# Kernel optimization log

Measured on AMD Instinct MI355X. Metric: run time of the kernel, lower is better.

## Reference

```python
import jax, jax.numpy as jnp
import numpy as np

N_GROUPS = 32
N_HEADS = 8
GN_EPS = 1e-5


def setup_inputs() -> dict:
    key = jax.random.key(0)
    k1, k2, k3 = jax.random.split(key, 3)
    B, C, H, W = 8, 512, 32, 32
    x = jax.random.normal(k1, (B, C, H, W), dtype=jnp.float32)
    gn_w = jnp.ones((C,), dtype=jnp.float32)
    gn_b = jnp.zeros((C,), dtype=jnp.float32)
    qkv_w = jax.random.normal(k2, (3 * C, C), dtype=jnp.float32) * 0.02
    qkv_b = jnp.zeros((3 * C,), dtype=jnp.float32)
    proj_w = jax.random.normal(k3, (C, C), dtype=jnp.float32) * 0.02
    proj_b = jnp.zeros((C,), dtype=jnp.float32)
    return {"x": x, "gn_w": gn_w, "gn_b": gn_b, "qkv_w": qkv_w,
            "qkv_b": qkv_b, "proj_w": proj_w, "proj_b": proj_b}


def reference(x, gn_w, gn_b, qkv_w, qkv_b, proj_w, proj_b):
    b, c, h, w = x.shape
    t = h * w
    xf = x.reshape(b, c, t)

    # GroupNorm(32, C) over (channel-group, spatial) dims
    xg = xf.reshape(b, N_GROUPS, (c // N_GROUPS) * t)
    mean = jnp.mean(xg, axis=-1, keepdims=True)
    var = jnp.var(xg, axis=-1, keepdims=True)
    normed = ((xg - mean) * jax.lax.rsqrt(var + GN_EPS)).reshape(b, c, t)
    normed = normed * gn_w[None, :, None] + gn_b[None, :, None]

    # 1x1 Conv1d -> matmul over channel dim
    qkv = jnp.einsum('oc,bct->bot', qkv_w, normed) + qkv_b[None, :, None]
    q, k, v = jnp.split(qkv, 3, axis=1)  # each [b, c, t]

    ch = c // N_HEADS
    scale = 1.0 / np.sqrt(np.sqrt(ch)).astype(np.float32)
    q = (q * scale).reshape(b * N_HEADS, ch, t)
    k = (k * scale).reshape(b * N_HEADS, ch, t)
    v = v.reshape(b * N_HEADS, ch, t)

    weight = jnp.einsum('bct,bcs->bts', q, k)
    weight = jax.nn.softmax(weight.astype(jnp.float32), axis=-1).astype(q.dtype)
    a = jnp.einsum('bts,bcs->bct', weight, v).reshape(b, c, t)

    # residual + 1x1 Conv2d projection
    out = jnp.einsum('oc,bct->bot', proj_w, xf + a) + proj_b[None, :, None]
    return out.reshape(b, -1, h, w)
```

## Files before the change

kernel.cpp:

```cpp
#include <hip/hip_runtime.h>

constexpr int B = 8;
constexpr int C = 512;
constexpr int T = 1024;
constexpr int CPG = 16;
constexpr int NH = 8;
constexpr int CH = 64;
constexpr float GN_EPS = 1e-5f;
constexpr float QSCALE = 0.18033688011112042f;

typedef __attribute__((ext_vector_type(4))) float f32x4;
typedef __attribute__((ext_vector_type(8))) short bf16x8;
typedef __attribute__((ext_vector_type(4))) short bf16x4;

__device__ inline short f2bf(float f) {
  union { float f; unsigned u; } v; v.f = f;
  unsigned r = (v.u + 0x7FFFu + ((v.u >> 16) & 1u)) >> 16;
  return (short)r;
}

__device__ inline unsigned cvt_pk_bf16(float a, float b) {
  unsigned r;
  asm("v_cvt_pk_bf16_f32 %0, %1, %2" : "=v"(r) : "v"(a), "v"(b));
  return r;
}

#define GLOAD16(gsrc, ldst) __builtin_amdgcn_global_load_lds( \
    (const __attribute__((address_space(1))) unsigned int*)(gsrc), \
    (__attribute__((address_space(3))) unsigned int*)(ldst), 16, 0, 0)

__global__ __launch_bounds__(256)
void wconv_kernel(const float* __restrict__ qw, const float* __restrict__ pw,
                  short* __restrict__ qwb, short* __restrict__ pwb) {
  const int idx = blockIdx.x * 256 + threadIdx.x;
  constexpr int QW4 = 3 * C * C / 4;
  float4 v;
  short* dst;
  if (idx < QW4) {
    v = ((const float4*)qw)[idx];
    dst = qwb + (size_t)idx * 4;
  } else {
    v = ((const float4*)pw)[idx - QW4];
    dst = pwb + (size_t)(idx - QW4) * 4;
  }
  bf16x4 o;
  o[0] = f2bf(v.x); o[1] = f2bf(v.y); o[2] = f2bf(v.z); o[3] = f2bf(v.w);
  *(bf16x4*)dst = o;
}

__global__ __launch_bounds__(256)
void gn_kernel(const float* __restrict__ x, const float* __restrict__ gw,
               const float* __restrict__ gb, short* __restrict__ out) {
  const int b = blockIdx.x >> 5;
  const int g = blockIdx.x & 31;
  const float* xp = x + (size_t)(b * C + g * CPG) * T;
  const float4* x4 = (const float4*)xp;
  float s = 0.f, ss = 0.f;
  for (int i = threadIdx.x; i < CPG * T / 4; i += 256) {
    float4 v = x4[i];
    s  += v.x + v.y + v.z + v.w;
    ss += v.x * v.x + v.y * v.y + v.z * v.z + v.w * v.w;
  }
  #pragma unroll
  for (int o = 32; o; o >>= 1) {
    s  += __shfl_down(s, o);
    ss += __shfl_down(ss, o);
  }
  __shared__ float rs[4], rss[4];
  __shared__ float sm, sr;
  const int wid = threadIdx.x >> 6;
  if ((threadIdx.x & 63) == 0) { rs[wid] = s; rss[wid] = ss; }
  __syncthreads();
  if (threadIdx.x == 0) {
    float ts  = rs[0] + rs[1] + rs[2] + rs[3];
    float tss = rss[0] + rss[1] + rss[2] + rss[3];
    constexpr float inv_n = 1.f / (CPG * T);
    float mean = ts * inv_n;
    float var = tss * inv_n - mean * mean;
    sm = mean;
    sr = rsqrtf(var + GN_EPS);
  }
  __syncthreads();
  const float mean = sm, rstd = sr;

  const int tid = threadIdx.x;
  const int cl = tid >> 4;
  const int t4 = (tid & 15) * 4;
  const float cw = gw[g * CPG + cl] * rstd;
  const float cb = gb[g * CPG + cl] - mean * cw;
  __shared__ short tile[64][20];
  const int tr = tid >> 2;
  const int cq = (tid & 3) * 4;
  for (int t0 = 0; t0 < T; t0 += 64) {
    float4 v = x4[(cl * T + t0 + t4) >> 2];
    tile[t4 + 0][cl] = f2bf(v.x * cw + cb);
    tile[t4 + 1][cl] = f2bf(v.y * cw + cb);
    tile[t4 + 2][cl] = f2bf(v.z * cw + cb);
    tile[t4 + 3][cl] = f2bf(v.w * cw + cb);
    __syncthreads();
    *(bf16x4*)&out[((size_t)(b * T + t0 + tr)) * C + g * CPG + cq] =
        *(const bf16x4*)&tile[tr][cq];
    __syncthreads();
  }
}

__global__ __launch_bounds__(256)
void qkv_gemm(const short* __restrict__ Wb, const float* __restrict__ bias,
              const short* __restrict__ Xn, short* __restrict__ qb,
              short* __restrict__ kb, short* __restrict__ vb) {
  const int bid = blockIdx.x;
  const int b = bid & 7;
  const int rem = bid >> 3;
  const int o0 = (rem % 12) * 128;
  const int t0 = (rem / 12) * 128;
  const bool swap = (o0 >= 2 * C);
  __shared__ short Asm[128 * 64];
  __shared__ short Bsm[128 * 64];
  const int tid = threadIdx.x;
  const int wv = tid >> 6, lane = tid & 63;
  const int l15 = lane & 15, l4 = lane >> 4;
  const int wr = (wv >> 1) * 64, wc = (wv & 1) * 64;

  const short* gA[4]; const short* gB[4];
  char* lA[4]; char* lB[4];
  #pragma unroll
  for (int p = 0; p < 4; ++p) {
    const int off = p * 256 + tid;
    const int row = off >> 3;
    const int col = (off & 7) ^ (row & 7);
    gA[p] = Wb + (size_t)(o0 + row) * C + col * 8;
    gB[p] = Xn + ((size_t)b * T + t0 + row) * C + col * 8;
    lA[p] = (char*)Asm + (size_t)(p * 256 + (tid & ~63)) * 16;
    lB[p] = (char*)Bsm + (size_t)(p * 256 + (tid & ~63)) * 16;
  }

  f32x4 acc[4][4];
  #pragma unroll
  for (int i = 0; i < 4; ++i)
    #pragma unroll
    for (int j = 0; j < 4; ++j) acc[i][j] = f32x4{0.f, 0.f, 0.f, 0.f};

  for (int k0 = 0; k0 < C; k0 += 64) {
    #pragma unroll
    for (int p = 0; p < 4; ++p) {
      GLOAD16(gA[p] + k0, lA[p]);
      GLOAD16(gB[p] + k0, lB[p]);
    }
    __syncthreads();
    #pragma unroll
    for (int kk = 0; kk < 2; ++kk) {
      bf16x8 af[4], bfr[4];
      #pragma unroll
      for (int i = 0; i < 4; ++i) {
        const int sw = ((kk << 2) | l4) ^ (l15 & 7);
        af[i]  = *(const bf16x8*)&Asm[(wr + i * 16 + l15) * 64 + sw * 8];
        bfr[i] = *(const bf16x8*)&Bsm[(wc + i * 16 + l15) * 64 + sw * 8];
      }
      if (!swap) {
        #pragma unroll
        for (int fi = 0; fi < 4; ++fi)
          #pragma unroll
          for (int nj = 0; nj < 4; ++nj)
            acc[fi][nj] = __builtin_amdgcn_mfma_f32_16x16x32_bf16(
                af[fi], bfr[nj], acc[fi][nj], 0, 0, 0);
      } else {
        #pragma unroll
        for (int nj = 0; nj < 4; ++nj)
          #pragma unroll
          for (int fi = 0; fi < 4; ++fi)
            acc[nj][fi] = __builtin_amdgcn_mfma_f32_16x16x32_bf16(
                bfr[nj], af[fi], acc[nj][fi], 0, 0, 0);
      }
    }
    __syncthreads();
  }

  if (!swap) {
    short* dst = (o0 < C) ? qb : kb;
    const float sc = (o0 < C) ? QSCALE : 1.0f;
    #pragma unroll
    for (int fi = 0; fi < 4; ++fi) {
      const int ob = o0 + wr + fi * 16 + l4 * 4;
      const int bh = b * NH + ((ob >> 6) & 7);
      const int cb_ = ob & 63;
      #pragma unroll
      for (int nj = 0; nj < 4; ++nj) {
        const int tg = t0 + wc + nj * 16 + l15;
        bf16x4 pk;
        #pragma unroll
        for (int r = 0; r < 4; ++r)
          pk[r] = f2bf((acc[fi][nj][r] + bias[ob + r]) * sc);
        *(bf16x4*)&dst[((size_t)bh * T + tg) * CH + cb_] = pk;
      }
    }
  } else {
    #pragma unroll
    for (int fi = 0; fi < 4; ++fi) {
      const int ob = o0 + wr + fi * 16 + l15;
      const int bh = b * NH + ((ob >> 6) & 7);
      const int cb_ = ob & 63;
      const float bo = bias[ob];
      #pragma unroll
      for (int nj = 0; nj < 4; ++nj) {
        const int tg = t0 + wc + nj * 16 + l4 * 4;
        bf16x4 pk;
        #pragma unroll
        for (int r = 0; r < 4; ++r)
          pk[r] = f2bf(acc[nj][fi][r] + bo);
        *(bf16x4*)&vb[((size_t)bh * CH + cb_) * T + tg] = pk;
      }
    }
  }
}

__global__ __launch_bounds__(256)
void attn_kernel(const short* __restrict__ qb, const short* __restrict__ kb,
                 const short* __restrict__ vb, const float* __restrict__ x,
                 short* __restrict__ res) {
  const int bh = blockIdx.x & 63;
  const int tile = blockIdx.x >> 6;
  const int b = bh >> 3, h = bh & 7;
  const int t0 = tile * 128;
  const int tid = threadIdx.x;
  const int wv = tid >> 6;
  const int lane = tid & 63;
  const int l15 = lane & 15;
  const int l4 = lane >> 4;

  const short* qh = qb + (size_t)bh * T * CH;
  const short* kh = kb + (size_t)bh * T * CH;
  const short* vh = vb + (size_t)bh * CH * T;

  __shared__ short kt[2][64][64];
  __shared__ short vt[2][64][64];
  __shared__ short pl[4][2][16][64];
  short* plw = &pl[wv][0][0][0];

  const int sl_row[2] = { (0 * 256 + tid) >> 3, (1 * 256 + tid) >> 3 };
  const int sl_blk[2] = { (tid & 7) ^ (sl_row[0] & 7), (tid & 7) ^ (sl_row[1] & 7) };
  const int sl_lds[2] = { (0 * 256 + (tid & ~63)) * 8, (1 * 256 + (tid & ~63)) * 8 };

  bf16x8 qf[2][2];
  #pragma unroll
  for (int nj = 0; nj < 2; ++nj)
    #pragma unroll
    for (int ks = 0; ks < 2; ++ks)
      qf[nj][ks] = *(const bf16x8*)
          &qh[(size_t)(t0 + wv * 32 + nj * 16 + l15) * CH + ks * 32 + l4 * 8];

  f32x4 acc_o[2][4];
  #pragma unroll
  for (int nj = 0; nj < 2; ++nj)
    #pragma unroll
    for (int ct = 0; ct < 4; ++ct) acc_o[nj][ct] = f32x4{0.f, 0.f, 0.f, 0.f};
  float lsum[2] = {0.f, 0.f};

  #pragma unroll
  for (int p = 0; p < 2; ++p) {
    GLOAD16(kh + (size_t)sl_row[p] * CH + sl_blk[p] * 8, (char*)&kt[0][0][0] + sl_lds[p] * 2);
    GLOAD16(vh + (size_t)sl_row[p] * T + sl_blk[p] * 8, (char*)&vt[0][0][0] + sl_lds[p] * 2);
  }

  for (int it = 0; it < 16; ++it) {
    const int cur = it & 1;
    __syncthreads();
    if (it < 15) {
      const int s1 = (it + 1) * 64;
      #pragma unroll
      for (int p = 0; p < 2; ++p) {
        GLOAD16(kh + (size_t)(s1 + sl_row[p]) * CH + sl_blk[p] * 8,
                (char*)&kt[cur ^ 1][0][0] + sl_lds[p] * 2);
        GLOAD16(vh + (size_t)sl_row[p] * T + s1 + sl_blk[p] * 8,
                (char*)&vt[cur ^ 1][0][0] + sl_lds[p] * 2);
      }
    }
    const short* ktc = &kt[cur][0][0];
    const short* vtc = &vt[cur][0][0];

    f32x4 accs[2][4];
    #pragma unroll
    for (int nj = 0; nj < 2; ++nj)
      #pragma unroll
      for (int nt = 0; nt < 4; ++nt) accs[nj][nt] = f32x4{0.f, 0.f, 0.f, 0.f};
    __builtin_amdgcn_s_setprio(1);
    #pragma unroll
    for (int ks = 0; ks < 2; ++ks) {
      #pragma unroll
      for (int nt = 0; nt < 4; ++nt) {
        bf16x8 kf = *(const bf16x8*)
            &ktc[(nt * 16 + l15) * 64 + (((ks << 2) | l4) ^ (l15 & 7)) * 8];
        accs[0][nt] = __builtin_amdgcn_mfma_f32_16x16x32_bf16(kf, qf[0][ks], accs[0][nt], 0, 0, 0);
        accs[1][nt] = __builtin_amdgcn_mfma_f32_16x16x32_bf16(kf, qf[1][ks], accs[1][nt], 0, 0, 0);
      }
    }
    __builtin_amdgcn_s_setprio(0);

    f32x4 p4[2][4];
    #pragma unroll
    for (int nj = 0; nj < 2; ++nj) {
      #pragma unroll
      for (int nt = 0; nt < 4; ++nt)
        #pragma unroll
        for (int r = 0; r < 4; ++r)
          p4[nj][nt][r] = __builtin_amdgcn_exp2f(accs[nj][nt][r]);
      f32x4 sv;
      #pragma unroll
      for (int r = 0; r < 4; ++r)
        sv[r] = (p4[nj][0][r] + p4[nj][1][r]) + (p4[nj][2][r] + p4[nj][3][r]);
      lsum[nj] += (sv[0] + sv[1]) + (sv[2] + sv[3]);
      #pragma unroll
      for (int nt = 0; nt < 4; ++nt) {
        uint2 w;
        w.x = cvt_pk_bf16(p4[nj][nt][0], p4[nj][nt][1]);
        w.y = cvt_pk_bf16(p4[nj][nt][2], p4[nj][nt][3]);
        *(uint2*)&plw[nj * 1024 + l15 * 64 +
                      ((nt * 2 + (l4 >> 1)) ^ (l15 & 7)) * 8 + (l4 & 1) * 4] = w;
      }
    }

    __builtin_amdgcn_s_setprio(1);
    #pragma unroll
    for (int ks = 0; ks < 2; ++ks) {
      const int psl = (((ks << 2) | l4) ^ (l15 & 7)) * 8;
      bf16x8 pf0 = *(const bf16x8*)&plw[l15 * 64 + psl];
      bf16x8 pf1 = *(const bf16x8*)&plw[1024 + l15 * 64 + psl];
      #pragma unroll
      for (int ct = 0; ct < 4; ++ct) {
        bf16x8 vf = *(const bf16x8*)
            &vtc[(ct * 16 + l15) * 64 + (((ks << 2) | l4) ^ (l15 & 7)) * 8];
        acc_o[0][ct] = __builtin_amdgcn_mfma_f32_16x16x32_bf16(vf, pf0, acc_o[0][ct], 0, 0, 0);
        acc_o[1][ct] = __builtin_amdgcn_mfma_f32_16x16x32_bf16(vf, pf1, acc_o[1][ct], 0, 0, 0);
      }
    }
    __builtin_amdgcn_s_setprio(0);
  }

  #pragma unroll
  for (int nj = 0; nj < 2; ++nj) {
    float l = lsum[nj];
    l += __shfl_xor(l, 16);
    l += __shfl_xor(l, 32);
    const float inv = 1.f / l;
    const int trow = t0 + wv * 32 + nj * 16 + l15;
    #pragma unroll
    for (int ct = 0; ct < 4; ++ct) {
      const int cbase = h * CH + ct * 16 + l4 * 4;
      bf16x4 pk;
      #pragma unroll
      for (int r = 0; r < 4; ++r) {
        const float xv = x[((size_t)(b * C + cbase + r)) * T + trow];
        pk[r] = f2bf(acc_o[nj][ct][r] * inv + xv);
      }
      *(bf16x4*)&res[((size_t)(b * T + trow)) * C + cbase] = pk;
    }
  }
}

__global__ __launch_bounds__(256)
void proj_gemm(const short* __restrict__ Wp, const float* __restrict__ bias,
               const short* __restrict__ Rs, float* __restrict__ out) {
  const int bid = blockIdx.x;
  const int b = bid & 7;
  const int rem = bid >> 3;
  const int o0 = (rem % 4) * 128;
  const int t0 = (rem / 4) * 128;
  __shared__ short Asm[128 * 64];
  __shared__ short Bsm[128 * 64];
  const int tid = threadIdx.x;
  const int wv = tid >> 6, lane = tid & 63;
  const int l15 = lane & 15, l4 = lane >> 4;
  const int wr = (wv >> 1) * 64, wc = (wv & 1) * 64;

  const short* gA[4]; const short* gB[4];
  char* lA[4]; char* lB[4];
  #pragma unroll
  for (int p = 0; p < 4; ++p) {
    const int off = p * 256 + tid;
    const int row = off >> 3;
    const int col = (off & 7) ^ (row & 7);
    gA[p] = Wp + (size_t)(o0 + row) * C + col * 8;
    gB[p] = Rs + ((size_t)b * T + t0 + row) * C + col * 8;
    lA[p] = (char*)Asm + (size_t)(p * 256 + (tid & ~63)) * 16;
    lB[p] = (char*)Bsm + (size_t)(p * 256 + (tid & ~63)) * 16;
  }

  f32x4 acc[4][4];
  #pragma unroll
  for (int i = 0; i < 4; ++i)
    #pragma unroll
    for (int j = 0; j < 4; ++j) acc[i][j] = f32x4{0.f, 0.f, 0.f, 0.f};

  for (int k0 = 0; k0 < C; k0 += 64) {
    #pragma unroll
    for (int p = 0; p < 4; ++p) {
      GLOAD16(gA[p] + k0, lA[p]);
      GLOAD16(gB[p] + k0, lB[p]);
    }
    __syncthreads();
    #pragma unroll
    for (int kk = 0; kk < 2; ++kk) {
      bf16x8 af[4], bfr[4];
      #pragma unroll
      for (int i = 0; i < 4; ++i) {
        const int sw = ((kk << 2) | l4) ^ (l15 & 7);
        af[i]  = *(const bf16x8*)&Asm[(wr + i * 16 + l15) * 64 + sw * 8];
        bfr[i] = *(const bf16x8*)&Bsm[(wc + i * 16 + l15) * 64 + sw * 8];
      }
      #pragma unroll
      for (int nj = 0; nj < 4; ++nj)
        #pragma unroll
        for (int fi = 0; fi < 4; ++fi)
          acc[nj][fi] = __builtin_amdgcn_mfma_f32_16x16x32_bf16(
              bfr[nj], af[fi], acc[nj][fi], 0, 0, 0);
    }
    __syncthreads();
  }

  #pragma unroll
  for (int fi = 0; fi < 4; ++fi) {
    const int o = o0 + wr + fi * 16 + l15;
    const float bo = bias[o];
    #pragma unroll
    for (int nj = 0; nj < 4; ++nj) {
      const int tg = t0 + wc + nj * 16 + l4 * 4;
      f32x4 vo;
      #pragma unroll
      for (int r = 0; r < 4; ++r) vo[r] = acc[nj][fi][r] + bo;
      *(f32x4*)&out[((size_t)(b * C + o)) * T + tg] = vo;
    }
  }
}

extern "C" void kernel_launch(void* const* d_in, const int* in_sizes, int n_in,
                              void* d_out, int out_size, void* d_ws, size_t ws_size,
                              hipStream_t stream) {
  const float* x      = (const float*)d_in[0];
  const float* gn_w   = (const float*)d_in[1];
  const float* gn_b   = (const float*)d_in[2];
  const float* qkv_w  = (const float*)d_in[3];
  const float* qkv_b  = (const float*)d_in[4];
  const float* proj_w = (const float*)d_in[5];
  const float* proj_b = (const float*)d_in[6];
  float* out = (float*)d_out;

  constexpr size_t MB = 1 << 20;
  char* w = (char*)d_ws;
  short* normed = (short*)w;
  short* qbuf   = (short*)(w + 8 * MB);
  short* kbuf   = (short*)(w + 16 * MB);
  short* vbuf   = (short*)(w + 24 * MB);
  short* resb   = (short*)(w + 32 * MB);
  short* qwb    = (short*)(w + 40 * MB);
  short* pwb    = (short*)(w + 40 * MB + (size_t)3 * C * C * 2);

  wconv_kernel<<<dim3(1024), 256, 0, stream>>>(qkv_w, proj_w, qwb, pwb);
  gn_kernel<<<dim3(B * 32), 256, 0, stream>>>(x, gn_w, gn_b, normed);
  qkv_gemm<<<dim3(768), 256, 0, stream>>>(qwb, qkv_b, normed, qbuf, kbuf, vbuf);
  attn_kernel<<<dim3(B * NH * (T / 128)), 256, 0, stream>>>(qbuf, kbuf, vbuf, x, resb);
  proj_gemm<<<dim3(256), 256, 0, stream>>>(pwb, proj_b, resb, out);
}
```

Baseline: 90.92 us.

## Load K/V fragments directly from global into registers, drop LDS staging

The attention kernel no longer stages K and V tiles in double-buffered shared memory with async global-to-LDS loads and a per-iteration barrier. Each wave now loads its MFMA operand fragments for K and V straight from global memory into registers. This removes the LDS traffic and the __syncthreads. In exchange, every wave fetches the same K/V data separately, so there is more global and L2 traffic and no explicit prefetch to overlap load latency.

```diff
diff --git a/kernel.cpp b/kernel.cpp
--- a/kernel.cpp
+++ b/kernel.cpp
@@ -228,17 +228,11 @@
   const int l4 = lane >> 4;
 
   const short* qh = qb + (size_t)bh * T * CH;
-  const short* kh = kb + (size_t)bh * T * CH;
-  const short* vh = vb + (size_t)bh * CH * T;
-
-  __shared__ short kt[2][64][64];
-  __shared__ short vt[2][64][64];
+  const short* kbase = kb + (size_t)bh * T * CH + (size_t)l15 * CH + l4 * 8;
+  const short* vbase = vb + (size_t)bh * CH * T + (size_t)l15 * T + l4 * 8;
+
   __shared__ short pl[4][2][16][64];
   short* plw = &pl[wv][0][0][0];
-
-  const int sl_row[2] = { (0 * 256 + tid) >> 3, (1 * 256 + tid) >> 3 };
-  const int sl_blk[2] = { (tid & 7) ^ (sl_row[0] & 7), (tid & 7) ^ (sl_row[1] & 7) };
-  const int sl_lds[2] = { (0 * 256 + (tid & ~63)) * 8, (1 * 256 + (tid & ~63)) * 8 };
 
   bf16x8 qf[2][2];
   #pragma unroll
@@ -255,27 +249,15 @@
     for (int ct = 0; ct < 4; ++ct) acc_o[nj][ct] = f32x4{0.f, 0.f, 0.f, 0.f};
   float lsum[2] = {0.f, 0.f};
 
-  #pragma unroll
-  for (int p = 0; p < 2; ++p) {
-    GLOAD16(kh + (size_t)sl_row[p] * CH + sl_blk[p] * 8, (char*)&kt[0][0][0] + sl_lds[p] * 2);
-    GLOAD16(vh + (size_t)sl_row[p] * T + sl_blk[p] * 8, (char*)&vt[0][0][0] + sl_lds[p] * 2);
-  }
-
   for (int it = 0; it < 16; ++it) {
-    const int cur = it & 1;
-    __syncthreads();
-    if (it < 15) {
-      const int s1 = (it + 1) * 64;
-      #pragma unroll
-      for (int p = 0; p < 2; ++p) {
-        GLOAD16(kh + (size_t)(s1 + sl_row[p]) * CH + sl_blk[p] * 8,
-                (char*)&kt[cur ^ 1][0][0] + sl_lds[p] * 2);
-        GLOAD16(vh + (size_t)sl_row[p] * T + s1 + sl_blk[p] * 8,
-                (char*)&vt[cur ^ 1][0][0] + sl_lds[p] * 2);
-      }
-    }
-    const short* ktc = &kt[cur][0][0];
-    const short* vtc = &vt[cur][0][0];
+    const int s0 = it * 64;
+
+    bf16x8 kf[2][4];
+    #pragma unroll
+    for (int ks = 0; ks < 2; ++ks)
+      #pragma unroll
+      for (int nt = 0; nt < 4; ++nt)
+        kf[ks][nt] = *(const bf16x8*)&kbase[(size_t)(s0 + nt * 16) * CH + ks * 32];
 
     f32x4 accs[2][4];
     #pragma unroll
@@ -287,13 +269,18 @@
     for (int ks = 0; ks < 2; ++ks) {
       #pragma unroll
       for (int nt = 0; nt < 4; ++nt) {
-        bf16x8 kf = *(const bf16x8*)
-            &ktc[(nt * 16 + l15) * 64 + (((ks << 2) | l4) ^ (l15 & 7)) * 8];
-        accs[0][nt] = __builtin_amdgcn_mfma_f32_16x16x32_bf16(kf, qf[0][ks], accs[0][nt], 0, 0, 0);
-        accs[1][nt] = __builtin_amdgcn_mfma_f32_16x16x32_bf16(kf, qf[1][ks], accs[1][nt], 0, 0, 0);
+        accs[0][nt] = __builtin_amdgcn_mfma_f32_16x16x32_bf16(kf[ks][nt], qf[0][ks], accs[0][nt], 0, 0, 0);
+        accs[1][nt] = __builtin_amdgcn_mfma_f32_16x16x32_bf16(kf[ks][nt], qf[1][ks], accs[1][nt], 0, 0, 0);
       }
     }
     __builtin_amdgcn_s_setprio(0);
+
+    bf16x8 vf[2][4];
+    #pragma unroll
+    for (int ks = 0; ks < 2; ++ks)
+      #pragma unroll
+      for (int ct = 0; ct < 4; ++ct)
+        vf[ks][ct] = *(const bf16x8*)&vbase[(size_t)(ct * 16) * T + s0 + ks * 32];
 
     f32x4 p4[2][4];
     #pragma unroll
@@ -326,10 +313,8 @@
       bf16x8 pf1 = *(const bf16x8*)&plw[1024 + l15 * 64 + psl];
       #pragma unroll
       for (int ct = 0; ct < 4; ++ct) {
-        bf16x8 vf = *(const bf16x8*)
-            &vtc[(ct * 16 + l15) * 64 + (((ks << 2) | l4) ^ (l15 & 7)) * 8];
-        acc_o[0][ct] = __builtin_amdgcn_mfma_f32_16x16x32_bf16(vf, pf0, acc_o[0][ct], 0, 0, 0);
-        acc_o[1][ct] = __builtin_amdgcn_mfma_f32_16x16x32_bf16(vf, pf1, acc_o[1][ct], 0, 0, 0);
+        acc_o[0][ct] = __builtin_amdgcn_mfma_f32_16x16x32_bf16(vf[ks][ct], pf0, acc_o[0][ct], 0, 0, 0);
+        acc_o[1][ct] = __builtin_amdgcn_mfma_f32_16x16x32_bf16(vf[ks][ct], pf1, acc_o[1][ct], 0, 0, 0);
       }
     }
     __builtin_amdgcn_s_setprio(0);
```

Result: slower. 125.2 us (+37.7%).
